# Performance work log

Measured on AMD Instinct MI355X. Metric: run time of the kernel, lower is better.

The kernel has to match this reference:

```python
import jax, jax.numpy as jnp
import numpy as np

B, D, T, H, K = 16, 1024, 1024, 1024, 2  # batch, in_channels, seq_len, hidden_size, kernel_size


def setup_inputs() -> dict:
    key = jax.random.key(0)
    k1, k2, k3 = jax.random.split(key, 3)
    inputs = jax.random.normal(k1, (B, D, T), dtype=jnp.float32)
    # Conv1D kernel in OIH layout: [3H, D, K]; scaled to keep gates in a sane range
    conv_w = jax.random.normal(k2, (3 * H, D, K), dtype=jnp.float32) / np.float32(np.sqrt(D * K))
    conv_b = jax.random.normal(k3, (3 * H,), dtype=jnp.float32) * 0.01
    return {"inputs": inputs, "conv_w": conv_w, "conv_b": conv_b}


def reference(inputs, conv_w, conv_b):
    # inputs: [B, D, T] (channels_first, as in the keras call signature)
    # Causal conv: left-pad time by K-1, then VALID conv -> [B, 3H, T]
    padded = jnp.pad(inputs, ((0, 0), (0, 0), (K - 1, 0)))
    gates = jax.lax.conv_general_dilated(
        padded, conv_w, window_strides=(1,), padding="VALID",
        dimension_numbers=("NCH", "OIH", "NCH"))
    gates = gates + conv_b[None, :, None]
    gates = jnp.transpose(gates, (0, 2, 1))  # [B, T, 3H]
    z = jnp.tanh(gates[..., :H])
    f = jax.nn.sigmoid(gates[..., H:2 * H])
    o = jax.nn.sigmoid(gates[..., 2 * H:])

    # fo-pooling linear recurrence: c_t = f_t * c_{t-1} + (1 - f_t) * z_t, c_0 = 0
    zf = (jnp.transpose(z, (1, 0, 2)), jnp.transpose(f, (1, 0, 2)))  # time-major [T, B, H]

    def step(c, zf_t):
        z_t, f_t = zf_t
        c_new = f_t * c + (1.0 - f_t) * z_t
        return c_new, c_new

    c0 = jnp.zeros((B, H), dtype=inputs.dtype)
    _, c_seq = jax.lax.scan(step, c0, zf)
    c_seq = jnp.transpose(c_seq, (1, 0, 2))  # [B, T, H]
    h_seq = o * c_seq
    return c_seq, h_seq
```

## Files before the change

### kernel.cpp

```cpp
#include <hip/hip_runtime.h>

#define Bsz 16
#define Dch 1024
#define Tsz 1024
#define Hsz 1024
#define Mtot (Bsz*Tsz)
#define K2   (2*Dch)
#define Ntot (3*Hsz)
#define NCH  16
#define CL   64

typedef __attribute__((ext_vector_type(8))) short bf16x8;
typedef __attribute__((ext_vector_type(4))) float f32x4;

__device__ __forceinline__ unsigned short f2bf(float x) {
    unsigned u = __float_as_uint(x);
    u += 0x7FFFu + ((u >> 16) & 1u);
    return (unsigned short)(u >> 16);
}
__device__ __forceinline__ float bf2f(unsigned short s) {
    return __uint_as_float(((unsigned)s) << 16);
}

#define GLOAD_LDS16(gp, lp) \
    __builtin_amdgcn_global_load_lds((const __attribute__((address_space(1))) void*)(gp), \
                                     (__attribute__((address_space(3))) void*)(lp), 16, 0, 0)

__global__ __launch_bounds__(256)
void prep(const float* __restrict__ x, unsigned short* __restrict__ a2,
          const float* __restrict__ w, unsigned short* __restrict__ wb) {
    __shared__ float Xs[64][66];
    int bid = blockIdx.x;
    int tid = threadIdx.x;
    if (bid >= 4096) {
        int i0 = (bid - 4096) * 256 + tid;
        #pragma unroll
        for (int k = 0; k < 4; k++) {
            int i = i0 + k * (1536 * 256);
            float4 v = ((const float4*)w)[i];
            ushort4 r;
            r.x = f2bf(v.x); r.y = f2bf(v.y); r.z = f2bf(v.z); r.w = f2bf(v.w);
            ((ushort4*)wb)[i] = r;
        }
        return;
    }
    int b   = bid >> 8;
    int tt0 = ((bid >> 4) & 15) << 6;
    int dd0 = (bid & 15) << 6;
    int colt = tid & 63, rowq = tid >> 6;
    const size_t xbase = (size_t)b * (Dch * Tsz);
    #pragma unroll
    for (int r = 0; r < 16; r++) {
        int dd = r * 4 + rowq;
        Xs[dd][1 + colt] = x[xbase + (size_t)(dd0 + dd) * Tsz + tt0 + colt];
    }
    if (tid < 64) {
        Xs[tid][0] = (tt0 == 0) ? 0.f : x[xbase + (size_t)(dd0 + tid) * Tsz + tt0 - 1];
    }
    __syncthreads();
    #pragma unroll
    for (int r = 0; r < 16; r++) {
        int tr = r * 4 + rowq;
        int dc = colt;
        float v0 = Xs[dc][tr];
        float v1 = Xs[dc][tr + 1];
        unsigned pack = (unsigned)f2bf(v0) | ((unsigned)f2bf(v1) << 16);
        int m = (b << 10) + tt0 + tr;
        ((unsigned*)a2)[(size_t)m * (K2 / 2) + dd0 + dc] = pack;
    }
}

__global__ __launch_bounds__(256)
void gemm_gates(const unsigned short* __restrict__ A, const unsigned short* __restrict__ Bt,
                const float* __restrict__ bias,
                float* __restrict__ zc, float* __restrict__ fh, unsigned short* __restrict__ ob) {
    __shared__ __align__(16) unsigned short As[128 * 64];
    __shared__ __align__(16) unsigned short Bs2[128 * 64];
    int tid = threadIdx.x;
    int n0 = blockIdx.x << 7;
    int m0 = blockIdx.y << 7;
    int wave = tid >> 6, lane = tid & 63;
    int wm = wave & 1, wn = wave >> 1;
    int lm = lane & 15, q = lane >> 4;

    int lrow = lane >> 3, lchunk = lane & 7;
    int gch  = lchunk ^ lrow;
    const unsigned short* Ag = A  + (size_t)(m0 + wave * 32 + lrow) * K2 + gch * 8;
    const unsigned short* Bg = Bt + (size_t)(n0 + wave * 32 + lrow) * K2 + gch * 8;

    f32x4 acc[4][4] = {};
    for (int kb = 0; kb < K2; kb += 64) {
        #pragma unroll
        for (int j = 0; j < 4; j++) {
            int rbase = wave * 32 + j * 8;
            GLOAD_LDS16(Ag + (size_t)j * 8 * K2 + kb, &As[rbase * 64]);
            GLOAD_LDS16(Bg + (size_t)j * 8 * K2 + kb, &Bs2[rbase * 64]);
        }
        __syncthreads();
        #pragma unroll
        for (int ks = 0; ks < 64; ks += 32) {
            bf16x8 af[4], bfr[4];
            int cs = ks >> 3;
            int sw = (lm & 7);
            #pragma unroll
            for (int i = 0; i < 4; i++)
                af[i] = *(bf16x8*)&As[(wm * 64 + i * 16 + lm) * 64 + (((cs + q) ^ sw) << 3)];
            #pragma unroll
            for (int j = 0; j < 4; j++)
                bfr[j] = *(bf16x8*)&Bs2[(wn * 64 + j * 16 + lm) * 64 + (((cs + q) ^ sw) << 3)];
            #pragma unroll
            for (int i = 0; i < 4; i++)
                #pragma unroll
                for (int j = 0; j < 4; j++)
                    acc[i][j] = __builtin_amdgcn_mfma_f32_16x16x32_bf16(af[i], bfr[j], acc[i][j], 0, 0, 0);
        }
        __syncthreads();
    }
    int gt = n0 >> 10;
    #pragma unroll
    for (int i = 0; i < 4; i++) {
        int mrow = m0 + wm * 64 + i * 16 + q * 4;
        #pragma unroll
        for (int j = 0; j < 4; j++) {
            int n = n0 + wn * 64 + j * 16 + lm;
            float bv = bias[n];
            int hcol = n & 1023;
            #pragma unroll
            for (int r = 0; r < 4; r++) {
                float g = acc[i][j][r] + bv;
                size_t idx = (size_t)(mrow + r) * Hsz + hcol;
                if (gt == 0) {
                    float e = __expf(2.f * g);
                    zc[idx] = __fdividef(e - 1.f, e + 1.f);
                } else {
                    float s = __fdividef(1.f, 1.f + __expf(-g));
                    if (gt == 1) fh[idx] = s;
                    else         ob[idx] = f2bf(s);
                }
            }
        }
    }
}

__global__ __launch_bounds__(256)
void scan1(const float* __restrict__ zc, const float* __restrict__ fh,
           float* __restrict__ Aw, float* __restrict__ Bw) {
    int blk = blockIdx.x;
    int hb = blk & 1, ch = (blk >> 1) & 15, b = blk >> 5;
    int h = hb * 512 + threadIdx.x * 2;
    size_t base = ((size_t)b << 20) + ((size_t)(ch * CL) << 10) + h;
    float ax = 1.f, ay = 1.f, bx = 0.f, by = 0.f;
    #pragma unroll 8
    for (int s = 0; s < CL; s++) {
        size_t idx = base + ((size_t)s << 10);
        float2 z = *(const float2*)&zc[idx];
        float2 f = *(const float2*)&fh[idx];
        ax *= f.x; ay *= f.y;
        bx = z.x + f.x * (bx - z.x);
        by = z.y + f.y * (by - z.y);
    }
    int o = (ch * Bsz + b) * Hsz + h;
    *(float2*)&Aw[o] = make_float2(ax, ay);
    *(float2*)&Bw[o] = make_float2(bx, by);
}

__global__ __launch_bounds__(256)
void scan3(float* __restrict__ zc, float* __restrict__ fh,
           const unsigned short* __restrict__ ob,
           const float* __restrict__ Aw, const float* __restrict__ Bw) {
    int blk = blockIdx.x;
    int hb = blk & 1, ch = (blk >> 1) & 15, b = blk >> 5;
    int h = hb * 512 + threadIdx.x * 2;
    float cx = 0.f, cy = 0.f;
    for (int cp = 0; cp < ch; cp++) {
        int o = (cp * Bsz + b) * Hsz + h;
        float2 A = *(const float2*)&Aw[o];
        float2 B = *(const float2*)&Bw[o];
        cx = A.x * cx + B.x;
        cy = A.y * cy + B.y;
    }
    size_t base = ((size_t)b << 20) + ((size_t)(ch * CL) << 10) + h;
    #pragma unroll 8
    for (int s = 0; s < CL; s++) {
        size_t idx = base + ((size_t)s << 10);
        float2 z = *(const float2*)&zc[idx];
        float2 f = *(const float2*)&fh[idx];
        unsigned ov = *(const unsigned*)&ob[idx];
        cx = z.x + f.x * (cx - z.x);
        cy = z.y + f.y * (cy - z.y);
        *(float2*)&zc[idx] = make_float2(cx, cy);
        float ox = bf2f((unsigned short)(ov & 0xFFFF));
        float oy = bf2f((unsigned short)(ov >> 16));
        *(float2*)&fh[idx] = make_float2(ox * cx, oy * cy);
    }
}

extern "C" void kernel_launch(void* const* d_in, const int* in_sizes, int n_in,
                              void* d_out, int out_size, void* d_ws, size_t ws_size,
                              hipStream_t stream) {
    const float* x    = (const float*)d_in[0];
    const float* w    = (const float*)d_in[1];
    const float* bias = (const float*)d_in[2];
    float* zc = (float*)d_out;
    float* fh = (float*)d_out + (size_t)Mtot * Hsz;
    unsigned short* a2 = (unsigned short*)d_ws;
    unsigned short* wb = a2 + (size_t)Mtot * K2;
    unsigned short* ob = wb + (size_t)Ntot * K2;
    float* Aw = (float*)(ob + (size_t)Mtot * Hsz);
    float* Bw = Aw + NCH * Bsz * Hsz;

    hipLaunchKernelGGL(prep, dim3(5632), dim3(256), 0, stream, x, a2, w, wb);
    hipLaunchKernelGGL(gemm_gates, dim3(24, 128), dim3(256), 0, stream, a2, wb, bias, zc, fh, ob);
    hipLaunchKernelGGL(scan1, dim3(512), dim3(256), 0, stream, zc, fh, Aw, Bw);
    hipLaunchKernelGGL(scan3, dim3(512), dim3(256), 0, stream, zc, fh, ob, Aw, Bw);
}
```

Before: 510.7 us.

## Fuse two-pass chunked scan into single-pass decoupled-lookback scan kernel

Replaces the scan1/scan3 pair with one kernel in which blocks take ordered tickets and pass each chunk's carry to the next chunk through flag-tagged atomic slots. Each block keeps its z and f values in registers, packed as fp16, so the second pass no longer reads them again from global memory. The output gate is now stored as fp16 instead of bf16, and the chunk count doubles to 32 with 32 steps each. This removes one full read of z and f plus a kernel launch, but makes the carry propagation serial across chunks and adds fp16 rounding of z and f, which may hurt accuracy.

```diff
diff --git a/kernel.cpp b/kernel.cpp
--- a/kernel.cpp
+++ b/kernel.cpp
@@ -7,8 +7,9 @@
 #define Mtot (Bsz*Tsz)
 #define K2   (2*Dch)
 #define Ntot (3*Hsz)
-#define NCH  16
-#define CL   64
+#define NCH  32
+#define CL   32
+#define NSEQ 32
 
 typedef __attribute__((ext_vector_type(8))) short bf16x8;
 typedef __attribute__((ext_vector_type(4))) float f32x4;
@@ -18,8 +19,13 @@
     u += 0x7FFFu + ((u >> 16) & 1u);
     return (unsigned short)(u >> 16);
 }
-__device__ __forceinline__ float bf2f(unsigned short s) {
-    return __uint_as_float(((unsigned)s) << 16);
+__device__ __forceinline__ unsigned short f2h(float x) {
+    _Float16 h = (_Float16)x;
+    return __builtin_bit_cast(unsigned short, h);
+}
+__device__ __forceinline__ float h2f(unsigned short u) {
+    _Float16 h = __builtin_bit_cast(_Float16, u);
+    return (float)h;
 }
 
 #define GLOAD_LDS16(gp, lp) \
@@ -73,7 +79,7 @@
 __global__ __launch_bounds__(256)
 void gemm_gates(const unsigned short* __restrict__ A, const unsigned short* __restrict__ Bt,
                 const float* __restrict__ bias,
-                float* __restrict__ zc, float* __restrict__ fh, unsigned short* __restrict__ ob) {
+                float* __restrict__ zc, float* __restrict__ fh, unsigned short* __restrict__ og) {
     __shared__ __align__(16) unsigned short As[128 * 64];
     __shared__ __align__(16) unsigned short Bs2[128 * 64];
     int tid = threadIdx.x;
@@ -135,62 +141,79 @@
                 } else {
                     float s = __fdividef(1.f, 1.f + __expf(-g));
                     if (gt == 1) fh[idx] = s;
-                    else         ob[idx] = f2bf(s);
+                    else         og[idx] = f2h(s);
                 }
             }
         }
     }
 }
 
-__global__ __launch_bounds__(256)
-void scan1(const float* __restrict__ zc, const float* __restrict__ fh,
-           float* __restrict__ Aw, float* __restrict__ Bw) {
-    int blk = blockIdx.x;
-    int hb = blk & 1, ch = (blk >> 1) & 15, b = blk >> 5;
-    int h = hb * 512 + threadIdx.x * 2;
+__global__ __launch_bounds__(256, 3)
+void qrnn_scan(float* __restrict__ zc, float* __restrict__ fh,
+               const unsigned short* __restrict__ og,
+               unsigned long long* __restrict__ pub, int* __restrict__ ticket) {
+    __shared__ int s_vb;
+    if (threadIdx.x == 0) s_vb = atomicAdd(ticket, 1);
+    __syncthreads();
+    int v   = s_vb;
+    int seq = v & (NSEQ - 1);
+    int ch  = v >> 5;
+    int b = seq >> 1, hb = seq & 1;
+    int j2 = threadIdx.x * 2;
+    int h  = hb * 512 + j2;
     size_t base = ((size_t)b << 20) + ((size_t)(ch * CL) << 10) + h;
+
     float ax = 1.f, ay = 1.f, bx = 0.f, by = 0.f;
-    #pragma unroll 8
+    uint2 pk[CL];
+    #pragma unroll
     for (int s = 0; s < CL; s++) {
         size_t idx = base + ((size_t)s << 10);
         float2 z = *(const float2*)&zc[idx];
         float2 f = *(const float2*)&fh[idx];
-        ax *= f.x; ay *= f.y;
-        bx = z.x + f.x * (bx - z.x);
-        by = z.y + f.y * (by - z.y);
-    }
-    int o = (ch * Bsz + b) * Hsz + h;
-    *(float2*)&Aw[o] = make_float2(ax, ay);
-    *(float2*)&Bw[o] = make_float2(bx, by);
-}
-
-__global__ __launch_bounds__(256)
-void scan3(float* __restrict__ zc, float* __restrict__ fh,
-           const unsigned short* __restrict__ ob,
-           const float* __restrict__ Aw, const float* __restrict__ Bw) {
-    int blk = blockIdx.x;
-    int hb = blk & 1, ch = (blk >> 1) & 15, b = blk >> 5;
-    int h = hb * 512 + threadIdx.x * 2;
+        ax *= f.x; bx = z.x + f.x * (bx - z.x);
+        ay *= f.y; by = z.y + f.y * (by - z.y);
+        pk[s].x = (unsigned)f2h(z.x) | ((unsigned)f2h(f.x) << 16);
+        pk[s].y = (unsigned)f2h(z.y) | ((unsigned)f2h(f.y) << 16);
+    }
+
     float cx = 0.f, cy = 0.f;
-    for (int cp = 0; cp < ch; cp++) {
-        int o = (cp * Bsz + b) * Hsz + h;
-        float2 A = *(const float2*)&Aw[o];
-        float2 B = *(const float2*)&Bw[o];
-        cx = A.x * cx + B.x;
-        cy = A.y * cy + B.y;
-    }
-    size_t base = ((size_t)b << 20) + ((size_t)(ch * CL) << 10) + h;
-    #pragma unroll 8
+    unsigned long long* slot = pub + ((size_t)seq * NCH + ch) * 512;
+    if (ch > 0) {
+        unsigned long long* ps = slot - 512;
+        unsigned long long v0, v1;
+        for (;;) {
+            v0 = __hip_atomic_load(&ps[j2], __ATOMIC_RELAXED, __HIP_MEMORY_SCOPE_AGENT);
+            if (v0 >> 32) break;
+            __builtin_amdgcn_s_sleep(4);
+        }
+        for (;;) {
+            v1 = __hip_atomic_load(&ps[j2 + 1], __ATOMIC_RELAXED, __HIP_MEMORY_SCOPE_AGENT);
+            if (v1 >> 32) break;
+            __builtin_amdgcn_s_sleep(4);
+        }
+        cx = __uint_as_float((unsigned)v0);
+        cy = __uint_as_float((unsigned)v1);
+    }
+    if (ch < NCH - 1) {
+        unsigned long long px = (1ull << 32) | (unsigned long long)__float_as_uint(ax * cx + bx);
+        unsigned long long py = (1ull << 32) | (unsigned long long)__float_as_uint(ay * cy + by);
+        __hip_atomic_store(&slot[j2],     px, __ATOMIC_RELAXED, __HIP_MEMORY_SCOPE_AGENT);
+        __hip_atomic_store(&slot[j2 + 1], py, __ATOMIC_RELAXED, __HIP_MEMORY_SCOPE_AGENT);
+    }
+
+    #pragma unroll
     for (int s = 0; s < CL; s++) {
         size_t idx = base + ((size_t)s << 10);
-        float2 z = *(const float2*)&zc[idx];
-        float2 f = *(const float2*)&fh[idx];
-        unsigned ov = *(const unsigned*)&ob[idx];
-        cx = z.x + f.x * (cx - z.x);
-        cy = z.y + f.y * (cy - z.y);
+        unsigned ov = *(const unsigned*)&og[idx];
+        float zx = h2f((unsigned short)(pk[s].x & 0xFFFF));
+        float fx = h2f((unsigned short)(pk[s].x >> 16));
+        float zy = h2f((unsigned short)(pk[s].y & 0xFFFF));
+        float fy = h2f((unsigned short)(pk[s].y >> 16));
+        cx = zx + fx * (cx - zx);
+        cy = zy + fy * (cy - zy);
         *(float2*)&zc[idx] = make_float2(cx, cy);
-        float ox = bf2f((unsigned short)(ov & 0xFFFF));
-        float oy = bf2f((unsigned short)(ov >> 16));
+        float ox = h2f((unsigned short)(ov & 0xFFFF));
+        float oy = h2f((unsigned short)(ov >> 16));
         *(float2*)&fh[idx] = make_float2(ox * cx, oy * cy);
     }
 }
@@ -205,12 +228,12 @@
     float* fh = (float*)d_out + (size_t)Mtot * Hsz;
     unsigned short* a2 = (unsigned short*)d_ws;
     unsigned short* wb = a2 + (size_t)Mtot * K2;
-    unsigned short* ob = wb + (size_t)Ntot * K2;
-    float* Aw = (float*)(ob + (size_t)Mtot * Hsz);
-    float* Bw = Aw + NCH * Bsz * Hsz;
-
+    unsigned short* og = wb + (size_t)Ntot * K2;
+    unsigned long long* pub = (unsigned long long*)(og + (size_t)Mtot * Hsz);
+    int* ticket = (int*)(pub + (size_t)NSEQ * NCH * 512);
+
+    hipMemsetAsync(pub, 0, (size_t)NSEQ * NCH * 512 * 8 + 64, stream);
     hipLaunchKernelGGL(prep, dim3(5632), dim3(256), 0, stream, x, a2, w, wb);
-    hipLaunchKernelGGL(gemm_gates, dim3(24, 128), dim3(256), 0, stream, a2, wb, bias, zc, fh, ob);
-    hipLaunchKernelGGL(scan1, dim3(512), dim3(256), 0, stream, zc, fh, Aw, Bw);
-    hipLaunchKernelGGL(scan3, dim3(512), dim3(256), 0, stream, zc, fh, ob, Aw, Bw);
-}
+    hipLaunchKernelGGL(gemm_gates, dim3(24, 128), dim3(256), 0, stream, a2, wb, bias, zc, fh, og);
+    hipLaunchKernelGGL(qrnn_scan, dim3(Bsz * 2 * NCH), dim3(256), 0, stream, zc, fh, og, pub, ticket);
+}
```

After: 602.5 us. +18.0%, slower.
